# Kernel tuning notes

Measured on AMD Instinct MI355X. Metric: run time of the kernel, lower is better.

Reference implementation:

```python
import jax, jax.numpy as jnp
import numpy as np
import math

B, L, D_IN, D, H, NL, FF = 8, 1024, 32, 512, 8, 6, 64
DK = D // H

def _ln(x, g, b, eps=1e-5):
    m = jnp.mean(x, axis=-1, keepdims=True)
    v = jnp.mean((x - m) ** 2, axis=-1, keepdims=True)
    return (x - m) * jax.lax.rsqrt(v + eps) * g + b

def setup_inputs() -> dict:
    key = jax.random.key(0)
    ks = jax.random.split(key, 32)
    def nrm(k, shape, s=0.02):
        return jax.random.normal(k, shape, jnp.float32) * s
    x = jax.random.normal(ks[0], (B, L, D_IN), jnp.float32)
    mask = jnp.broadcast_to(jnp.tril(jnp.ones((L, L), jnp.int32))[None], (B, L, L))
    obs_time = jnp.arange(B * L, dtype=jnp.float32).reshape(B, L)
    inp = {
        "x": x, "mask": mask, "obs_time": obs_time,
        # embedding MLP: Linear(d_input,d) -> ReLU -> [Dropout] -> LayerNorm -> Linear(d,d)
        "emb_w1": nrm(ks[1], (D_IN, D)), "emb_b1": jnp.zeros((D,), jnp.float32),
        "emb_g": jnp.ones((D,), jnp.float32), "emb_beta": jnp.zeros((D,), jnp.float32),
        "emb_w2": nrm(ks[2], (D, D)), "emb_b2": jnp.zeros((D,), jnp.float32),
        # per-layer stacked params [NL, ...]
        "wq": nrm(ks[3], (NL, D, D)), "wk": nrm(ks[4], (NL, D, D)), "wv": nrm(ks[5], (NL, D, D)),
        "wo": nrm(ks[6], (NL, D, D)), "bo": jnp.zeros((NL, D), jnp.float32),
        "fw1": nrm(ks[7], (NL, D, FF)), "fb1": jnp.zeros((NL, FF), jnp.float32),
        "fw2": nrm(ks[8], (NL, FF, D)), "fb2": jnp.zeros((NL, D), jnp.float32),
        "g1": jnp.ones((NL, D), jnp.float32), "b1": jnp.zeros((NL, D), jnp.float32),
        "g2": jnp.ones((NL, D), jnp.float32), "b2": jnp.zeros((NL, D), jnp.float32),
    }
    return inp

def reference(x, mask, obs_time, emb_w1, emb_b1, emb_g, emb_beta, emb_w2, emb_b2,
              wq, wk, wv, wo, bo, fw1, fb1, fw2, fb2, g1, b1, g2, b2):
    # positional encoding: pe[...,0::2]=sin(t*div), pe[...,1::2]=cos(t*div)
    t = obs_time[..., None]  # [B,L,1]
    div = jnp.exp(jnp.arange(0, D, 2, dtype=jnp.float32) * (-math.log(10000.0) / D))
    pe = jnp.stack([jnp.sin(t * div), jnp.cos(t * div)], axis=-1).reshape(x.shape[0], x.shape[1], D)

    # embedding MLP (dropout = identity at eval)
    h = jax.nn.relu(x @ emb_w1 + emb_b1)
    h = _ln(h, emb_g, emb_beta)
    h = h @ emb_w2 + emb_b2
    h = h + pe

    Bx, Lx = h.shape[0], h.shape[1]
    scale = 1.0 / np.sqrt(DK).astype(np.float32)
    mask4 = (mask == 0)[:, None]  # [B,1,L,L]
    for i in range(NL):
        # self-attention
        q = (h @ wq[i]).reshape(Bx, Lx, H, DK).transpose(0, 2, 1, 3)  # bhld
        k = (h @ wk[i]).reshape(Bx, Lx, H, DK).transpose(0, 2, 1, 3)
        v = (h @ wv[i]).reshape(Bx, Lx, H, DK).transpose(0, 2, 1, 3)
        scores = jnp.einsum('bhqd,bhkd->bhqk', q, k) * scale
        scores = jnp.where(mask4, -jnp.inf, scores)
        attn = jax.nn.softmax(scores, axis=-1)
        o = jnp.einsum('bhqk,bhkd->bhqd', attn, v).transpose(0, 2, 1, 3).reshape(Bx, Lx, D)
        o = o @ wo[i] + bo[i]
        h = _ln(h + o, g1[i], b1[i])
        # feed-forward d -> 64 -> d
        f = jax.nn.relu(h @ fw1[i] + fb1[i]) @ fw2[i] + fb2[i]
        h = _ln(h + f, g2[i], b2[i])
    return h
```

## Files before the change

kernel.cpp:

```cpp
#include <hip/hip_runtime.h>
#include <math.h>

typedef unsigned short u16;
typedef unsigned int   u32;
typedef __bf16 bf16_t;
typedef bf16_t bf16x8 __attribute__((ext_vector_type(8)));
typedef float  f32x4  __attribute__((ext_vector_type(4)));
typedef u16    u16x8  __attribute__((ext_vector_type(8)));
typedef u16    u16x4  __attribute__((ext_vector_type(4)));

#define B_   8
#define L_   1024
#define DIN_ 32
#define D_   512
#define H_   8
#define NL_  6
#define FF_  64
#define M_   (B_*L_)
#define DD_  (D_*D_)

#define PE_COEF (-0.017988946039015984f)
#define SC2     (0.18033688011112042f)

__device__ __forceinline__ u16 f2bf(float f) {
  u32 u = __builtin_bit_cast(u32, f);
  u32 r = (u + 0x7FFFu + ((u >> 16) & 1u)) >> 16;
  return (u16)r;
}
__device__ __forceinline__ u16 f2bf_fast(float f) {
  u32 u = __builtin_bit_cast(u32, f);
  return (u16)((u + 0x8000u) >> 16);
}
__device__ __forceinline__ float bf2f(u16 v) {
  u32 u = ((u32)v) << 16;
  return __builtin_bit_cast(float, u);
}

#define GLOAD_LDS16(gp, lp) \
  __builtin_amdgcn_global_load_lds((const __attribute__((address_space(1))) u32*)(gp), \
                                   (__attribute__((address_space(3))) u32*)(lp), 16, 0, 0)

__device__ __forceinline__ float block_reduce_sum(float v, float* smem4) {
  #pragma unroll
  for (int off = 32; off > 0; off >>= 1) v += __shfl_down(v, off, 64);
  int wid = threadIdx.x >> 6;
  __syncthreads();
  if ((threadIdx.x & 63) == 0) smem4[wid] = v;
  __syncthreads();
  return smem4[0] + smem4[1] + smem4[2] + smem4[3];
}

__global__ __launch_bounds__(256) void transpose_k(const float* __restrict__ W, u16* __restrict__ Wt,
                                                   int K, int N, size_t in_zs, size_t out_zs) {
  __shared__ float tile[32][33];
  size_t mi = (size_t)blockIdx.z * in_zs;
  size_t mo = (size_t)blockIdx.z * out_zs;
  int k0 = blockIdx.y * 32, n0 = blockIdx.x * 32;
  int tx = threadIdx.x & 31, ty = threadIdx.x >> 5;
  #pragma unroll
  for (int i = 0; i < 4; ++i)
    tile[ty + i*8][tx] = W[mi + (size_t)(k0 + ty + i*8)*N + n0 + tx];
  __syncthreads();
  #pragma unroll
  for (int i = 0; i < 4; ++i)
    Wt[mo + (size_t)(n0 + ty + i*8)*K + k0 + tx] = f2bf(tile[tx][ty + i*8]);
}

__global__ __launch_bounds__(256) void emb1_ln_kernel(const float* __restrict__ x, const float* __restrict__ W1,
                               const float* __restrict__ b1, const float* __restrict__ g,
                               const float* __restrict__ beta, u16* __restrict__ outb) {
  __shared__ float xs[DIN_];
  __shared__ float red[4];
  int m = blockIdx.x;
  int tid = threadIdx.x;
  if (tid < DIN_) xs[tid] = x[m*DIN_ + tid];
  __syncthreads();
  float v[2];
  #pragma unroll
  for (int r = 0; r < 2; ++r) {
    int n = tid + r*256;
    float acc = b1[n];
    #pragma unroll
    for (int k = 0; k < DIN_; ++k) acc += xs[k] * W1[k*D_ + n];
    v[r] = fmaxf(acc, 0.f);
  }
  float mean = block_reduce_sum(v[0] + v[1], red) * (1.f/D_);
  float d0 = v[0] - mean, d1 = v[1] - mean;
  float var = block_reduce_sum(d0*d0 + d1*d1, red) * (1.f/D_);
  float rstd = rsqrtf(var + 1e-5f);
  outb[(size_t)m*D_ + tid]       = f2bf(d0*rstd*g[tid]       + beta[tid]);
  outb[(size_t)m*D_ + tid + 256] = f2bf(d1*rstd*g[tid + 256] + beta[tid + 256]);
}

__global__ __launch_bounds__(256) void add_ln_kernel(const float* __restrict__ hin, const u16* __restrict__ res,
                              const float* __restrict__ g, const float* __restrict__ b,
                              float* __restrict__ outf, u16* __restrict__ outb) {
  __shared__ float red[4];
  int m = blockIdx.x;
  int tid = threadIdx.x;
  float v0 = hin[(size_t)m*D_ + tid]       + bf2f(res[(size_t)m*D_ + tid]);
  float v1 = hin[(size_t)m*D_ + tid + 256] + bf2f(res[(size_t)m*D_ + tid + 256]);
  float mean = block_reduce_sum(v0 + v1, red) * (1.f/D_);
  float d0 = v0 - mean, d1 = v1 - mean;
  float var = block_reduce_sum(d0*d0 + d1*d1, red) * (1.f/D_);
  float rstd = rsqrtf(var + 1e-5f);
  float o0 = d0*rstd*g[tid]       + b[tid];
  float o1 = d1*rstd*g[tid + 256] + b[tid + 256];
  outf[(size_t)m*D_ + tid]       = o0;
  outf[(size_t)m*D_ + tid + 256] = o1;
  outb[(size_t)m*D_ + tid]       = f2bf(o0);
  outb[(size_t)m*D_ + tid + 256] = f2bf(o1);
}

template<int BM, int BN, int EPI, bool WF, bool WB>
__global__ __launch_bounds__(256) void mgemm(const u16* __restrict__ A, const u16* __restrict__ Bt,
                            const float* __restrict__ bias, const float* __restrict__ extra,
                            float* __restrict__ Cf, u16* __restrict__ Cb,
                            int M, int N, int K) {
  constexpr int NBUF = 3;
  constexpr int LPT = BM/64 + BN/64;
  __shared__ __align__(16) u16 As[NBUF][BM*32];
  __shared__ __align__(16) u16 Bs[NBUF][BN*32];
  const int WR = BM/2, WC = BN/2, MR = WR/16, NR = WC/16;
  int nx = gridDim.x;
  int nwg = nx * gridDim.y;
  int flat = blockIdx.y * nx + blockIdx.x;
  int wid = (flat & 7) * (nwg >> 3) + (flat >> 3);
  int bm = (wid / nx) * BM, bn = (wid % nx) * BN;
  int tid = threadIdx.x, w = tid >> 6, l = tid & 63;
  int wr = w >> 1, wc = w & 1;
  int lq = l & 15, lg = l >> 4;
  f32x4 acc[MR][NR];
  #pragma unroll
  for (int m = 0; m < MR; ++m)
    #pragma unroll
    for (int n = 0; n < NR; ++n) acc[m][n] = f32x4{0.f,0.f,0.f,0.f};

  int srow = w*16 + (l >> 2);
  int scol = (l & 3)*8;

  auto stage = [&](int t, int bi) {
    int k0 = t << 5;
    #pragma unroll
    for (int i = 0; i < BM/64; ++i)
      GLOAD_LDS16(A + (size_t)(bm + i*64 + srow)*K + k0 + scol, &As[bi][i*2048 + w*512]);
    #pragma unroll
    for (int i = 0; i < BN/64; ++i)
      GLOAD_LDS16(Bt + (size_t)(bn + i*64 + srow)*K + k0 + scol, &Bs[bi][i*2048 + w*512]);
  };

  int nk = K >> 5;
  stage(0, 0);
  if (nk > 1) stage(1, 1);
  int bi = 0;
  #pragma unroll 1
  for (int t = 0; t < nk; ++t) {
    if (t + 1 < nk) {
      if constexpr (LPT == 2)      asm volatile("s_waitcnt vmcnt(2)" ::: "memory");
      else if constexpr (LPT == 3) asm volatile("s_waitcnt vmcnt(3)" ::: "memory");
      else if constexpr (LPT == 4) asm volatile("s_waitcnt vmcnt(4)" ::: "memory");
      else                         asm volatile("s_waitcnt vmcnt(0)" ::: "memory");
    } else {
      asm volatile("s_waitcnt vmcnt(0)" ::: "memory");
    }
    __builtin_amdgcn_s_barrier();
    __builtin_amdgcn_sched_barrier(0);
    if (t + 2 < nk) {
      int b2 = bi + 2; if (b2 >= NBUF) b2 -= NBUF;
      stage(t + 2, b2);
    }
    bf16x8 af[MR], bfr[NR];
    #pragma unroll
    for (int m = 0; m < MR; ++m)
      af[m] = *(const bf16x8*)&As[bi][(wr*WR + m*16 + lq)*32 + lg*8];
    #pragma unroll
    for (int n = 0; n < NR; ++n)
      bfr[n] = *(const bf16x8*)&Bs[bi][(wc*WC + n*16 + lq)*32 + lg*8];
    #pragma unroll
    for (int m = 0; m < MR; ++m)
      #pragma unroll
      for (int n = 0; n < NR; ++n)
        acc[m][n] = __builtin_amdgcn_mfma_f32_16x16x32_bf16(af[m], bfr[n], acc[m][n], 0, 0, 0);
    bi = (bi + 1 == NBUF) ? 0 : bi + 1;
  }

  #pragma unroll
  for (int m = 0; m < MR; ++m) {
    #pragma unroll
    for (int n = 0; n < NR; ++n) {
      #pragma unroll
      for (int r = 0; r < 4; ++r) {
        int row = bm + wr*WR + m*16 + lg*4 + r;
        int col = bn + wc*WC + n*16 + lq;
        float v = acc[m][n][r];
        if (EPI & 1) v += bias[col];
        if (EPI & 2) v = fmaxf(v, 0.f);
        if (EPI & 4) {
          float fr  = __expf((float)(col & ~1) * PE_COEF);
          float arg = extra[row] * fr;
          v += (col & 1) ? cosf(arg) : sinf(arg);
        }
        if (WF) Cf[(size_t)row*N + col] = v;
        if (WB) Cb[(size_t)row*N + col] = f2bf(v);
      }
    }
  }
}

#define QS_ 1536
__global__ __launch_bounds__(256) void attn_kernel(const u16* __restrict__ Q, const u16* __restrict__ Kp,
                                                   const u16* __restrict__ V, u16* __restrict__ O) {
  __shared__ __align__(16) u16 Ks[2][64*72];
  __shared__ __align__(16) u16 Vt[2][64*72];
  __shared__ __align__(16) u16 Ps[4][16*72];
  int flat = blockIdx.y * 8 + blockIdx.x;
  int wid  = (flat & 7) * 64 + (flat >> 3);
  int pair = wid & 7, bh = wid >> 3;
  int b = bh >> 3, hh = bh & 7;
  int rowbase = b * L_, col0 = hh * 64;
  int tid = threadIdx.x, w = tid >> 6, l = tid & 63;
  int lq = l & 15, lg = l >> 4;

  int krow = tid >> 3, kseg = tid & 7;
  int vg = tid >> 5, vd2 = (tid & 31) * 2;

  u16x8 kr0, kr1;
  u32 vr[8];
  u16x8 oc16;
  #pragma unroll
  for (int i = 0; i < 8; ++i) oc16[i] = 0x3F80u;
  const bf16x8 onesA = __builtin_bit_cast(bf16x8, oc16);

  #define LOADKV(t) { \
    kr0 = *(const u16x8*)&Kp[(size_t)(rowbase + (t)*64 + krow)*QS_ + col0 + kseg*8]; \
    kr1 = *(const u16x8*)&Kp[(size_t)(rowbase + (t)*64 + krow + 32)*QS_ + col0 + kseg*8]; \
    _Pragma("unroll") \
    for (int i_ = 0; i_ < 8; ++i_) \
      vr[i_] = *(const u32*)&V[(size_t)(rowbase + (t)*64 + vg*8 + i_)*QS_ + col0 + vd2]; }

  LOADKV(0);

  #pragma unroll 1
  for (int half = 0; half < 2; ++half) {
    int qt = half ? (15 - pair) : pair;
    int qrow = rowbase + qt*64 + w*16 + lq;
    bf16x8 qa0 = *(const bf16x8*)&Q[(size_t)qrow*QS_ + col0 + lg*8];
    bf16x8 qa1 = *(const bf16x8*)&Q[(size_t)qrow*QS_ + col0 + 32 + lg*8];
    float m_s[4];
    f32x4 o[4], o4;
    #pragma unroll
    for (int r = 0; r < 4; ++r) m_s[r] = -1e30f;
    #pragma unroll
    for (int n = 0; n < 4; ++n) o[n] = f32x4{0.f,0.f,0.f,0.f};
    o4 = f32x4{0.f,0.f,0.f,0.f};

    #pragma unroll 1
    for (int kt = 0; kt <= qt; ++kt) {
      int buf = kt & 1;
      __syncthreads();
      *(u16x8*)&Ks[buf][krow*72 + kseg*8]        = kr0;
      *(u16x8*)&Ks[buf][(krow + 32)*72 + kseg*8] = kr1;
      {
        u16x8 vlo, vhi;
        #pragma unroll
        for (int i = 0; i < 8; ++i) { vlo[i] = (u16)(vr[i] & 0xffffu); vhi[i] = (u16)(vr[i] >> 16); }
        *(u16x8*)&Vt[buf][vd2*72 + vg*8]     = vlo;
        *(u16x8*)&Vt[buf][(vd2+1)*72 + vg*8] = vhi;
      }
      __syncthreads();
      int nt = (kt < qt) ? (kt + 1) : (half == 0 ? 0 : -1);
      if (nt >= 0) LOADKV(nt);

      f32x4 t4[4];
      __builtin_amdgcn_s_setprio(1);
      #pragma unroll
      for (int f = 0; f < 4; ++f) {
        bf16x8 k0 = *(const bf16x8*)&Ks[buf][(f*16 + lq)*72 + lg*8];
        bf16x8 k1 = *(const bf16x8*)&Ks[buf][(f*16 + lq)*72 + 32 + lg*8];
        f32x4 z = f32x4{0.f,0.f,0.f,0.f};
        z = __builtin_amdgcn_mfma_f32_16x16x32_bf16(qa0, k0, z, 0, 0, 0);
        z = __builtin_amdgcn_mfma_f32_16x16x32_bf16(qa1, k1, z, 0, 0, 0);
        #pragma unroll
        for (int r = 0; r < 4; ++r) t4[f][r] = z[r] * SC2;
      }
      __builtin_amdgcn_s_setprio(0);
      if (kt == qt) {
        #pragma unroll
        for (int f = 0; f < 4; ++f) {
          int kvg = f*16 + lq;
          #pragma unroll
          for (int r = 0; r < 4; ++r)
            if (kvg > w*16 + lg*4 + r) t4[f][r] = -1e30f;
        }
      }
      float tm[4];
      bool need = false;
      #pragma unroll
      for (int r = 0; r < 4; ++r) {
        float v = fmaxf(fmaxf(t4[0][r], t4[1][r]), fmaxf(t4[2][r], t4[3][r]));
        v = fmaxf(v, __shfl_xor(v, 1));
        v = fmaxf(v, __shfl_xor(v, 2));
        v = fmaxf(v, __shfl_xor(v, 4));
        v = fmaxf(v, __shfl_xor(v, 8));
        tm[r] = v;
        need = need || (v > m_s[r]);
      }
      if (__any(need)) {
        float corr[4];
        #pragma unroll
        for (int r = 0; r < 4; ++r) {
          float mn = fmaxf(m_s[r], tm[r]);
          corr[r] = __builtin_amdgcn_exp2f(m_s[r] - mn);
          m_s[r] = mn;
        }
        int bsrc = (lq >> 2)*16 + lq;
        float c0 = __shfl(corr[0], bsrc);
        float c1 = __shfl(corr[1], bsrc);
        float c2 = __shfl(corr[2], bsrc);
        float c3 = __shfl(corr[3], bsrc);
        float cb = (lq & 2) ? ((lq & 1) ? c3 : c2) : ((lq & 1) ? c1 : c0);
        #pragma unroll
        for (int n = 0; n < 4; ++n)
          #pragma unroll
          for (int r = 0; r < 4; ++r) o[n][r] *= cb;
        #pragma unroll
        for (int r = 0; r < 4; ++r) o4[r] *= cb;
      }
      #pragma unroll
      for (int r = 0; r < 4; ++r) {
        int prow = (lg*4 + r)*72;
        Ps[w][prow + lq]      = f2bf_fast(__builtin_amdgcn_exp2f(t4[0][r] - m_s[r]));
        Ps[w][prow + 16 + lq] = f2bf_fast(__builtin_amdgcn_exp2f(t4[1][r] - m_s[r]));
        Ps[w][prow + 32 + lq] = f2bf_fast(__builtin_amdgcn_exp2f(t4[2][r] - m_s[r]));
        Ps[w][prow + 48 + lq] = f2bf_fast(__builtin_amdgcn_exp2f(t4[3][r] - m_s[r]));
      }
      bf16x8 pB0 = *(const bf16x8*)&Ps[w][lq*72 + lg*8];
      bf16x8 pB1 = *(const bf16x8*)&Ps[w][lq*72 + 32 + lg*8];
      __builtin_amdgcn_s_setprio(1);
      o4 = __builtin_amdgcn_mfma_f32_16x16x32_bf16(onesA, pB0, o4, 0, 0, 0);
      o4 = __builtin_amdgcn_mfma_f32_16x16x32_bf16(onesA, pB1, o4, 0, 0, 0);
      #pragma unroll
      for (int n = 0; n < 4; ++n) {
        bf16x8 vA0 = *(const bf16x8*)&Vt[buf][(n*16 + lq)*72 + lg*8];
        bf16x8 vA1 = *(const bf16x8*)&Vt[buf][(n*16 + lq)*72 + 32 + lg*8];
        o[n] = __builtin_amdgcn_mfma_f32_16x16x32_bf16(vA0, pB0, o[n], 0, 0, 0);
        o[n] = __builtin_amdgcn_mfma_f32_16x16x32_bf16(vA1, pB1, o[n], 0, 0, 0);
      }
      __builtin_amdgcn_s_setprio(0);
    }
    float inv = 1.f / o4[0];
    #pragma unroll
    for (int n = 0; n < 4; ++n) {
      u16x4 pk;
      #pragma unroll
      for (int r = 0; r < 4; ++r) pk[r] = f2bf(o[n][r] * inv);
      *(u16x4*)&O[(size_t)(rowbase + qt*64 + w*16 + lq)*D_ + col0 + n*16 + lg*4] = pk;
    }
  }
  #undef LOADKV
}

extern "C" void kernel_launch(void* const* d_in, const int* in_sizes, int n_in,
                              void* d_out, int out_size, void* d_ws, size_t ws_size,
                              hipStream_t stream) {
  (void)in_sizes; (void)n_in; (void)out_size; (void)ws_size;
  const float* x      = (const float*)d_in[0];
  const float* obs    = (const float*)d_in[2];
  const float* emb_w1 = (const float*)d_in[3];
  const float* emb_b1 = (const float*)d_in[4];
  const float* emb_g  = (const float*)d_in[5];
  const float* emb_be = (const float*)d_in[6];
  const float* emb_w2 = (const float*)d_in[7];
  const float* emb_b2 = (const float*)d_in[8];
  const float* wq  = (const float*)d_in[9];
  const float* wk  = (const float*)d_in[10];
  const float* wv  = (const float*)d_in[11];
  const float* wo  = (const float*)d_in[12];
  const float* bo  = (const float*)d_in[13];
  const float* fw1 = (const float*)d_in[14];
  const float* fb1 = (const float*)d_in[15];
  const float* fw2 = (const float*)d_in[16];
  const float* fb2 = (const float*)d_in[17];
  const float* g1  = (const float*)d_in[18];
  const float* b1  = (const float*)d_in[19];
  const float* g2  = (const float*)d_in[20];
  const float* b2  = (const float*)d_in[21];
  float* out = (float*)d_out;

  float* hf  = (float*)d_ws;
  u16* hb    = (u16*)(hf + (size_t)M_*D_);
  u16* qkvb  = hb + (size_t)M_*D_;
  u16* ob    = qkvb + (size_t)M_*3*D_;
  u16* ofb   = ob + (size_t)M_*D_;
  u16* fhb   = ofb + (size_t)M_*D_;
  u16* qkvt  = fhb + (size_t)M_*FF_;
  u16* wot   = qkvt + (size_t)18*DD_;
  u16* ew2t  = wot + (size_t)6*DD_;
  u16* fw1t  = ew2t + (size_t)DD_;
  u16* fw2t  = fw1t + (size_t)6*D_*FF_;

  transpose_k<<<dim3(16,16,6), 256, 0, stream>>>(wq, qkvt,          512, 512, DD_, 3*(size_t)DD_);
  transpose_k<<<dim3(16,16,6), 256, 0, stream>>>(wk, qkvt + DD_,    512, 512, DD_, 3*(size_t)DD_);
  transpose_k<<<dim3(16,16,6), 256, 0, stream>>>(wv, qkvt + 2*DD_,  512, 512, DD_, 3*(size_t)DD_);
  transpose_k<<<dim3(16,16,6), 256, 0, stream>>>(wo, wot,           512, 512, DD_, DD_);
  transpose_k<<<dim3(16,16,1), 256, 0, stream>>>(emb_w2, ew2t,      512, 512, DD_, DD_);
  transpose_k<<<dim3(2,16,6),  256, 0, stream>>>(fw1, fw1t,         512,  64, (size_t)D_*FF_, (size_t)D_*FF_);
  transpose_k<<<dim3(16,2,6),  256, 0, stream>>>(fw2, fw2t,          64, 512, (size_t)D_*FF_, (size_t)D_*FF_);

  emb1_ln_kernel<<<M_, 256, 0, stream>>>(x, emb_w1, emb_b1, emb_g, emb_be, ob);
  mgemm<128,128,5,true,true><<<dim3(4,64), 256, 0, stream>>>(ob, ew2t, emb_b2, obs, hf, hb, M_, D_, D_);

  for (int i = 0; i < NL_; ++i) {
    mgemm<128,128,0,false,true><<<dim3(12,64), 256, 0, stream>>>(hb, qkvt + (size_t)i*3*DD_,
        nullptr, nullptr, nullptr, qkvb, M_, 3*D_, D_);
    attn_kernel<<<dim3(8, B_*H_), 256, 0, stream>>>(qkvb, qkvb + D_, qkvb + 2*D_, ob);
    mgemm<128,128,1,false,true><<<dim3(4,64), 256, 0, stream>>>(ob, wot + (size_t)i*DD_,
        bo + i*D_, nullptr, nullptr, ofb, M_, D_, D_);
    add_ln_kernel<<<M_, 256, 0, stream>>>(hf, ofb, g1 + i*D_, b1 + i*D_, hf, hb);
    mgemm<64,64,3,false,true><<<dim3(1,128), 256, 0, stream>>>(hb, fw1t + (size_t)i*D_*FF_,
        fb1 + i*FF_, nullptr, nullptr, fhb, M_, FF_, D_);
    mgemm<128,128,1,false,true><<<dim3(4,64), 256, 0, stream>>>(fhb, fw2t + (size_t)i*D_*FF_,
        fb2 + i*D_, nullptr, nullptr, ofb, M_, D_, FF_);
    add_ln_kernel<<<M_, 256, 0, stream>>>(hf, ofb, g2 + i*D_, b2 + i*D_,
        (i == NL_-1) ? out : hf, hb);
  }
}
```

Baseline: 848.3 us.

## Use BK=64 double-buffered GEMM, wave-per-row LayerNorm, and merged weight transposes

The GEMM mainloop moves from a 3-stage BK=32 pipeline to a 2-buffer BK=64 pipeline. It uses an XOR swizzle on LDS columns to avoid bank conflicts and issues two MFMAs per fragment pair per step. The add+LayerNorm kernel now gives each wavefront one row and reduces with shuffles only, so no block barriers are needed, and the grid shrinks by 4x. The five square weight transposes are merged into one launch, and the embedding LN drops a redundant barrier. The trade-off is that the shallower pipeline may expose more load latency per iteration.

```diff
diff --git a/kernel.cpp b/kernel.cpp
--- a/kernel.cpp
+++ b/kernel.cpp
@@ -40,14 +40,35 @@
   __builtin_amdgcn_global_load_lds((const __attribute__((address_space(1))) u32*)(gp), \
                                    (__attribute__((address_space(3))) u32*)(lp), 16, 0, 0)
 
-__device__ __forceinline__ float block_reduce_sum(float v, float* smem4) {
-  #pragma unroll
-  for (int off = 32; off > 0; off >>= 1) v += __shfl_down(v, off, 64);
-  int wid = threadIdx.x >> 6;
-  __syncthreads();
-  if ((threadIdx.x & 63) == 0) smem4[wid] = v;
-  __syncthreads();
-  return smem4[0] + smem4[1] + smem4[2] + smem4[3];
+__global__ __launch_bounds__(256) void transpose_all(const float* __restrict__ wq, const float* __restrict__ wk,
+                                                     const float* __restrict__ wv, const float* __restrict__ wo,
+                                                     const float* __restrict__ ew2,
+                                                     u16* __restrict__ qkvt, u16* __restrict__ wot,
+                                                     u16* __restrict__ ew2t) {
+  __shared__ float tile[32][33];
+  int z = blockIdx.z;
+  const float* src;
+  u16* dst;
+  if (z < 18) {
+    int grp = z / 6, i = z % 6;
+    src = (grp == 0 ? wq : grp == 1 ? wk : wv) + (size_t)i*DD_;
+    dst = qkvt + (size_t)i*3*DD_ + (size_t)grp*DD_;
+  } else if (z < 24) {
+    int i = z - 18;
+    src = wo + (size_t)i*DD_;
+    dst = wot + (size_t)i*DD_;
+  } else {
+    src = ew2; dst = ew2t;
+  }
+  int k0 = blockIdx.y * 32, n0 = blockIdx.x * 32;
+  int tx = threadIdx.x & 31, ty = threadIdx.x >> 5;
+  #pragma unroll
+  for (int i = 0; i < 4; ++i)
+    tile[ty + i*8][tx] = src[(size_t)(k0 + ty + i*8)*512 + n0 + tx];
+  __syncthreads();
+  #pragma unroll
+  for (int i = 0; i < 4; ++i)
+    dst[(size_t)(n0 + ty + i*8)*512 + k0 + tx] = f2bf(tile[tx][ty + i*8]);
 }
 
 __global__ __launch_bounds__(256) void transpose_k(const float* __restrict__ W, u16* __restrict__ Wt,
@@ -84,9 +105,21 @@
     for (int k = 0; k < DIN_; ++k) acc += xs[k] * W1[k*D_ + n];
     v[r] = fmaxf(acc, 0.f);
   }
-  float mean = block_reduce_sum(v[0] + v[1], red) * (1.f/D_);
+  float s = v[0] + v[1];
+  #pragma unroll
+  for (int off = 32; off > 0; off >>= 1) s += __shfl_down(s, off, 64);
+  int wid = tid >> 6;
+  if ((tid & 63) == 0) red[wid] = s;
+  __syncthreads();
+  float mean = (red[0] + red[1] + red[2] + red[3]) * (1.f/D_);
   float d0 = v[0] - mean, d1 = v[1] - mean;
-  float var = block_reduce_sum(d0*d0 + d1*d1, red) * (1.f/D_);
+  float vv = d0*d0 + d1*d1;
+  #pragma unroll
+  for (int off = 32; off > 0; off >>= 1) vv += __shfl_down(vv, off, 64);
+  __syncthreads();
+  if ((tid & 63) == 0) red[wid] = vv;
+  __syncthreads();
+  float var = (red[0] + red[1] + red[2] + red[3]) * (1.f/D_);
   float rstd = rsqrtf(var + 1e-5f);
   outb[(size_t)m*D_ + tid]       = f2bf(d0*rstd*g[tid]       + beta[tid]);
   outb[(size_t)m*D_ + tid + 256] = f2bf(d1*rstd*g[tid + 256] + beta[tid + 256]);
@@ -95,21 +128,34 @@
 __global__ __launch_bounds__(256) void add_ln_kernel(const float* __restrict__ hin, const u16* __restrict__ res,
                               const float* __restrict__ g, const float* __restrict__ b,
                               float* __restrict__ outf, u16* __restrict__ outb) {
-  __shared__ float red[4];
-  int m = blockIdx.x;
-  int tid = threadIdx.x;
-  float v0 = hin[(size_t)m*D_ + tid]       + bf2f(res[(size_t)m*D_ + tid]);
-  float v1 = hin[(size_t)m*D_ + tid + 256] + bf2f(res[(size_t)m*D_ + tid + 256]);
-  float mean = block_reduce_sum(v0 + v1, red) * (1.f/D_);
-  float d0 = v0 - mean, d1 = v1 - mean;
-  float var = block_reduce_sum(d0*d0 + d1*d1, red) * (1.f/D_);
-  float rstd = rsqrtf(var + 1e-5f);
-  float o0 = d0*rstd*g[tid]       + b[tid];
-  float o1 = d1*rstd*g[tid + 256] + b[tid + 256];
-  outf[(size_t)m*D_ + tid]       = o0;
-  outf[(size_t)m*D_ + tid + 256] = o1;
-  outb[(size_t)m*D_ + tid]       = f2bf(o0);
-  outb[(size_t)m*D_ + tid + 256] = f2bf(o1);
+  int w = threadIdx.x >> 6, lane = threadIdx.x & 63;
+  int m = blockIdx.x * 4 + w;
+  const float* hr = hin + (size_t)m*D_;
+  const u16*   rr = res + (size_t)m*D_;
+  float v[8];
+  float s = 0.f;
+  #pragma unroll
+  for (int i = 0; i < 8; ++i) {
+    int c = lane + i*64;
+    v[i] = hr[c] + bf2f(rr[c]);
+    s += v[i];
+  }
+  #pragma unroll
+  for (int off = 32; off > 0; off >>= 1) s += __shfl_xor(s, off, 64);
+  float mean = s * (1.f/D_);
+  float vs = 0.f;
+  #pragma unroll
+  for (int i = 0; i < 8; ++i) { v[i] -= mean; vs += v[i]*v[i]; }
+  #pragma unroll
+  for (int off = 32; off > 0; off >>= 1) vs += __shfl_xor(vs, off, 64);
+  float rstd = rsqrtf(vs * (1.f/D_) + 1e-5f);
+  #pragma unroll
+  for (int i = 0; i < 8; ++i) {
+    int c = lane + i*64;
+    float o = v[i]*rstd*g[c] + b[c];
+    outf[(size_t)m*D_ + c] = o;
+    outb[(size_t)m*D_ + c] = f2bf(o);
+  }
 }
 
 template<int BM, int BN, int EPI, bool WF, bool WB>
@@ -117,10 +163,10 @@
                             const float* __restrict__ bias, const float* __restrict__ extra,
                             float* __restrict__ Cf, u16* __restrict__ Cb,
                             int M, int N, int K) {
-  constexpr int NBUF = 3;
-  constexpr int LPT = BM/64 + BN/64;
-  __shared__ __align__(16) u16 As[NBUF][BM*32];
-  __shared__ __align__(16) u16 Bs[NBUF][BN*32];
+  constexpr int BK = 64;
+  constexpr int AI = BM/32, BI = BN/32;
+  __shared__ __align__(16) u16 As[2][BM*BK];
+  __shared__ __align__(16) u16 Bs[2][BN*BK];
   const int WR = BM/2, WC = BN/2, MR = WR/16, NR = WC/16;
   int nx = gridDim.x;
   int nwg = nx * gridDim.y;
@@ -130,58 +176,63 @@
   int tid = threadIdx.x, w = tid >> 6, l = tid & 63;
   int wr = w >> 1, wc = w & 1;
   int lq = l & 15, lg = l >> 4;
+  int lrow8 = l >> 3, lcol8 = l & 7;
   f32x4 acc[MR][NR];
   #pragma unroll
   for (int m = 0; m < MR; ++m)
     #pragma unroll
     for (int n = 0; n < NR; ++n) acc[m][n] = f32x4{0.f,0.f,0.f,0.f};
 
-  int srow = w*16 + (l >> 2);
-  int scol = (l & 3)*8;
-
   auto stage = [&](int t, int bi) {
-    int k0 = t << 5;
-    #pragma unroll
-    for (int i = 0; i < BM/64; ++i)
-      GLOAD_LDS16(A + (size_t)(bm + i*64 + srow)*K + k0 + scol, &As[bi][i*2048 + w*512]);
-    #pragma unroll
-    for (int i = 0; i < BN/64; ++i)
-      GLOAD_LDS16(Bt + (size_t)(bn + i*64 + srow)*K + k0 + scol, &Bs[bi][i*2048 + w*512]);
+    int k0 = t * BK;
+    #pragma unroll
+    for (int i = 0; i < AI; ++i) {
+      int row = (i*4 + w)*8 + lrow8;
+      int c8 = lcol8 ^ ((row & 1) << 2);
+      GLOAD_LDS16(A + (size_t)(bm + row)*K + k0 + c8*8, &As[bi][(i*4 + w)*512]);
+    }
+    #pragma unroll
+    for (int i = 0; i < BI; ++i) {
+      int row = (i*4 + w)*8 + lrow8;
+      int c8 = lcol8 ^ ((row & 1) << 2);
+      GLOAD_LDS16(Bt + (size_t)(bn + row)*K + k0 + c8*8, &Bs[bi][(i*4 + w)*512]);
+    }
   };
 
-  int nk = K >> 5;
+  int nk = K / BK;
   stage(0, 0);
-  if (nk > 1) stage(1, 1);
-  int bi = 0;
+  asm volatile("s_waitcnt vmcnt(0)" ::: "memory");
+  __builtin_amdgcn_s_barrier();
+  __builtin_amdgcn_sched_barrier(0);
+
+  int xh = lq & 1;
   #pragma unroll 1
   for (int t = 0; t < nk; ++t) {
+    int buf = t & 1;
+    if (t + 1 < nk) stage(t + 1, buf ^ 1);
+    bf16x8 af[MR][2], bf[NR][2];
+    #pragma unroll
+    for (int m = 0; m < MR; ++m)
+      #pragma unroll
+      for (int h = 0; h < 2; ++h)
+        af[m][h] = *(const bf16x8*)&As[buf][(wr*WR + m*16 + lq)*BK + (h ^ xh)*32 + lg*8];
+    #pragma unroll
+    for (int n = 0; n < NR; ++n)
+      #pragma unroll
+      for (int h = 0; h < 2; ++h)
+        bf[n][h] = *(const bf16x8*)&Bs[buf][(wc*WC + n*16 + lq)*BK + (h ^ xh)*32 + lg*8];
+    #pragma unroll
+    for (int m = 0; m < MR; ++m)
+      #pragma unroll
+      for (int n = 0; n < NR; ++n) {
+        acc[m][n] = __builtin_amdgcn_mfma_f32_16x16x32_bf16(af[m][0], bf[n][0], acc[m][n], 0, 0, 0);
+        acc[m][n] = __builtin_amdgcn_mfma_f32_16x16x32_bf16(af[m][1], bf[n][1], acc[m][n], 0, 0, 0);
+      }
     if (t + 1 < nk) {
-      if constexpr (LPT == 2)      asm volatile("s_waitcnt vmcnt(2)" ::: "memory");
-      else if constexpr (LPT == 3) asm volatile("s_waitcnt vmcnt(3)" ::: "memory");
-      else if constexpr (LPT == 4) asm volatile("s_waitcnt vmcnt(4)" ::: "memory");
-      else                         asm volatile("s_waitcnt vmcnt(0)" ::: "memory");
-    } else {
       asm volatile("s_waitcnt vmcnt(0)" ::: "memory");
-    }
-    __builtin_amdgcn_s_barrier();
-    __builtin_amdgcn_sched_barrier(0);
-    if (t + 2 < nk) {
-      int b2 = bi + 2; if (b2 >= NBUF) b2 -= NBUF;
-      stage(t + 2, b2);
-    }
-    bf16x8 af[MR], bfr[NR];
-    #pragma unroll
-    for (int m = 0; m < MR; ++m)
-      af[m] = *(const bf16x8*)&As[bi][(wr*WR + m*16 + lq)*32 + lg*8];
-    #pragma unroll
-    for (int n = 0; n < NR; ++n)
-      bfr[n] = *(const bf16x8*)&Bs[bi][(wc*WC + n*16 + lq)*32 + lg*8];
-    #pragma unroll
-    for (int m = 0; m < MR; ++m)
-      #pragma unroll
-      for (int n = 0; n < NR; ++n)
-        acc[m][n] = __builtin_amdgcn_mfma_f32_16x16x32_bf16(af[m], bfr[n], acc[m][n], 0, 0, 0);
-    bi = (bi + 1 == NBUF) ? 0 : bi + 1;
+      __builtin_amdgcn_s_barrier();
+      __builtin_amdgcn_sched_barrier(0);
+    }
   }
 
   #pragma unroll
@@ -399,13 +450,9 @@
   u16* fw1t  = ew2t + (size_t)DD_;
   u16* fw2t  = fw1t + (size_t)6*D_*FF_;
 
-  transpose_k<<<dim3(16,16,6), 256, 0, stream>>>(wq, qkvt,          512, 512, DD_, 3*(size_t)DD_);
-  transpose_k<<<dim3(16,16,6), 256, 0, stream>>>(wk, qkvt + DD_,    512, 512, DD_, 3*(size_t)DD_);
-  transpose_k<<<dim3(16,16,6), 256, 0, stream>>>(wv, qkvt + 2*DD_,  512, 512, DD_, 3*(size_t)DD_);
-  transpose_k<<<dim3(16,16,6), 256, 0, stream>>>(wo, wot,           512, 512, DD_, DD_);
-  transpose_k<<<dim3(16,16,1), 256, 0, stream>>>(emb_w2, ew2t,      512, 512, DD_, DD_);
-  transpose_k<<<dim3(2,16,6),  256, 0, stream>>>(fw1, fw1t,         512,  64, (size_t)D_*FF_, (size_t)D_*FF_);
-  transpose_k<<<dim3(16,2,6),  256, 0, stream>>>(fw2, fw2t,          64, 512, (size_t)D_*FF_, (size_t)D_*FF_);
+  transpose_all<<<dim3(16,16,25), 256, 0, stream>>>(wq, wk, wv, wo, emb_w2, qkvt, wot, ew2t);
+  transpose_k<<<dim3(2,16,6),  256, 0, stream>>>(fw1, fw1t, 512,  64, (size_t)D_*FF_, (size_t)D_*FF_);
+  transpose_k<<<dim3(16,2,6),  256, 0, stream>>>(fw2, fw2t,  64, 512, (size_t)D_*FF_, (size_t)D_*FF_);
 
   emb1_ln_kernel<<<M_, 256, 0, stream>>>(x, emb_w1, emb_b1, emb_g, emb_be, ob);
   mgemm<128,128,5,true,true><<<dim3(4,64), 256, 0, stream>>>(ob, ew2t, emb_b2, obs, hf, hb, M_, D_, D_);
@@ -416,12 +463,12 @@
     attn_kernel<<<dim3(8, B_*H_), 256, 0, stream>>>(qkvb, qkvb + D_, qkvb + 2*D_, ob);
     mgemm<128,128,1,false,true><<<dim3(4,64), 256, 0, stream>>>(ob, wot + (size_t)i*DD_,
         bo + i*D_, nullptr, nullptr, ofb, M_, D_, D_);
-    add_ln_kernel<<<M_, 256, 0, stream>>>(hf, ofb, g1 + i*D_, b1 + i*D_, hf, hb);
+    add_ln_kernel<<<M_/4, 256, 0, stream>>>(hf, ofb, g1 + i*D_, b1 + i*D_, hf, hb);
     mgemm<64,64,3,false,true><<<dim3(1,128), 256, 0, stream>>>(hb, fw1t + (size_t)i*D_*FF_,
         fb1 + i*FF_, nullptr, nullptr, fhb, M_, FF_, D_);
     mgemm<128,128,1,false,true><<<dim3(4,64), 256, 0, stream>>>(fhb, fw2t + (size_t)i*D_*FF_,
         fb2 + i*D_, nullptr, nullptr, ofb, M_, D_, FF_);
-    add_ln_kernel<<<M_, 256, 0, stream>>>(hf, ofb, g2 + i*D_, b2 + i*D_,
+    add_ln_kernel<<<M_/4, 256, 0, stream>>>(hf, ofb, g2 + i*D_, b2 + i*D_,
         (i == NL_-1) ? out : hf, hb);
   }
 }
```

Measured after the change: 866.7 us. 1.02x slower.
